# Kernel optimization log

Measured on AMD Instinct MI355X. Metric: run time of the kernel, lower is better.

## Reference

```python
import jax, jax.numpy as jnp
import numpy as np

D = 64        # GatedGraphConv out_channels
N_LAYERS = 5  # number of stacked convs


def setup_inputs() -> dict:
    key = jax.random.key(0)
    ks = jax.random.split(key, 16)
    N, E, G = 100000, 1600000, 64
    s = 0.1
    inp = {
        'conv_weight': jax.random.normal(ks[0], (N_LAYERS, D, D), jnp.float32) * s,
        'gru_w_ih':    jax.random.normal(ks[1], (N_LAYERS, 3 * D, D), jnp.float32) * s,
        'gru_w_hh':    jax.random.normal(ks[2], (N_LAYERS, 3 * D, D), jnp.float32) * s,
        'gru_b_ih':    jax.random.normal(ks[3], (N_LAYERS, 3 * D), jnp.float32) * s,
        'gru_b_hh':    jax.random.normal(ks[4], (N_LAYERS, 3 * D), jnp.float32) * s,
        'fc1_w': jax.random.normal(ks[5], (32, D), jnp.float32) * s,
        'fc1_b': jax.random.normal(ks[6], (32,), jnp.float32) * s,
        'fc2_w': jax.random.normal(ks[7], (16, 32), jnp.float32) * s,
        'fc2_b': jax.random.normal(ks[8], (16,), jnp.float32) * s,
        'fc3_w': jax.random.normal(ks[9], (1, 16), jnp.float32) * s,
        'fc3_b': jax.random.normal(ks[10], (1,), jnp.float32) * s,
        'edge_index': jax.random.randint(ks[11], (2, E), 0, N, jnp.int64 if jax.config.jax_enable_x64 else jnp.int32),
        'batch': jnp.sort(jax.random.randint(ks[12], (N,), 0, G, jnp.int32)),
        'num_nodes': N,
        'num_graphs': G,
    }
    return inp


def _gru_cell(m, h, w_ih, w_hh, b_ih, b_hh):
    # torch.nn.GRUCell math; m: [N,D] input, h: [N,D] hidden
    gi = m @ w_ih.T + b_ih   # [N, 3D]
    gh = h @ w_hh.T + b_hh   # [N, 3D]
    i_r, i_z, i_n = jnp.split(gi, 3, axis=1)
    h_r, h_z, h_n = jnp.split(gh, 3, axis=1)
    r = jax.nn.sigmoid(i_r + h_r)
    z = jax.nn.sigmoid(i_z + h_z)
    n = jnp.tanh(i_n + r * h_n)
    return (1.0 - z) * n + z * h


def reference(conv_weight, gru_w_ih, gru_w_hh, gru_b_ih, gru_b_hh,
              fc1_w, fc1_b, fc2_w, fc2_b, fc3_w, fc3_b,
              edge_index, batch, num_nodes, num_graphs):
    src, dst = edge_index[0], edge_index[1]  # source_to_target flow
    # initial node features: zeros [N,8] zero-padded to D by GatedGraphConv
    x0 = jnp.zeros((num_nodes, D), jnp.float32)

    def step(x, params):
        w, wih, whh, bih, bhh = params
        m = x @ w                                        # [N, D]
        agg = jax.ops.segment_sum(m[src], dst, num_segments=num_nodes)  # scatter-add
        return _gru_cell(agg, x, wih, whh, bih, bhh), None

    x, _ = jax.lax.scan(step, x0,
                        (conv_weight, gru_w_ih, gru_w_hh, gru_b_ih, gru_b_hh))

    # scatter_add pooling over batch -> [num_graphs, D]
    g = jax.ops.segment_sum(x, batch, num_segments=num_graphs)
    h = jax.nn.elu(g @ fc1_w.T + fc1_b)
    h = jax.nn.elu(h @ fc2_w.T + fc2_b)
    return h @ fc3_w.T + fc3_b  # [num_graphs, 1]
```

## Files before the change

kernel.cpp:

```cpp
#include <hip/hip_runtime.h>
#include <math.h>

typedef _Float16 f16x2 __attribute__((ext_vector_type(2)));
typedef _Float16 f16x4 __attribute__((ext_vector_type(4)));
typedef _Float16 f16x8 __attribute__((ext_vector_type(8)));
typedef float f32x4 __attribute__((ext_vector_type(4)));

#define CBITS 10
#define FCHUNK 4096
#define MATSZ 13056
#define SEGSZ 2176
__device__ __forceinline__ int woff(int row) { return 64 * row + 8 * (row >> 1); }

__device__ __forceinline__ float sigmoidf_(float v) {
  return 1.0f / (1.0f + __expf(-v));
}
__device__ __forceinline__ float tanhf_(float v) {
  v = fminf(fmaxf(v, -15.f), 15.f);
  float e = __expf(2.f * v);
  return (e - 1.f) / (e + 1.f);
}
__device__ __forceinline__ float eluf_(float v) { return v > 0.f ? v : (__expf(v) - 1.f); }

__global__ __launch_bounds__(256) void fuse_w_kernel(const float* __restrict__ conv_w,
                                                     const float* __restrict__ w_ih,
                                                     _Float16* __restrict__ wcS) {
  const int l = blockIdx.x >> 2;
  const int j0 = (blockIdx.x & 3) * 48;
  const float* W = conv_w + (size_t)l * 4096;
  const float* wi = w_ih + (size_t)l * 12288;
  _Float16* out = wcS + (size_t)l * MATSZ;
  __shared__ float sWt[64 * 68];
  __shared__ float sI[48 * 64];
  const int t = threadIdx.x;
  for (int i = t; i < 4096; i += 256) sWt[(i & 63) * 68 + (i >> 6)] = W[i];
  for (int i = t; i < 3072; i += 256) sI[i] = wi[j0 * 64 + i];
  __syncthreads();
#pragma unroll
  for (int r = 0; r < 3; ++r) {
    int u = t + 256 * r;
    int j = u >> 4, cg = (u & 15) * 4;
    float4 a = {0.f, 0.f, 0.f, 0.f};
    for (int k = 0; k < 64; ++k) {
      float4 w = *(const float4*)(sWt + k * 68 + cg);
      float s = sI[j * 64 + k];
      a.x += w.x * s; a.y += w.y * s; a.z += w.z * s; a.w += w.w * s;
    }
    int row = j0 + j;
    f16x4 hv;
    hv[0] = (_Float16)a.x; hv[1] = (_Float16)a.y;
    hv[2] = (_Float16)a.z; hv[3] = (_Float16)a.w;
    *(f16x4*)(out + woff(row) + cg) = hv;
  }
}

__global__ __launch_bounds__(256) void whh_prep_kernel(const float* __restrict__ whh,
                                                       _Float16* __restrict__ whhS) {
  int idx = blockIdx.x * 256 + threadIdx.x;
  if (idx >= 15360) return;
  int l = idx / 3072, rem = idx % 3072;
  int r = rem >> 4, c4 = (rem & 15) * 4;
  float4 v = *(const float4*)(whh + (size_t)l * 12288 + r * 64 + c4);
  f16x4 hv;
  hv[0] = (_Float16)v.x; hv[1] = (_Float16)v.y;
  hv[2] = (_Float16)v.z; hv[3] = (_Float16)v.w;
  *(f16x4*)(whhS + (size_t)l * MATSZ + woff(r) + c4) = hv;
}

__global__ __launch_bounds__(256) void bucket_hist_kernel(const int* __restrict__ dst,
                                                          int* __restrict__ bh, int E) {
  __shared__ int h[128];
  const int t = threadIdx.x;
  if (t < 128) h[t] = 0;
  __syncthreads();
  for (int e = blockIdx.x * 256 + t; e < E; e += gridDim.x * 256)
    atomicAdd(&h[dst[e] >> CBITS], 1);
  __syncthreads();
  if (t < 128 && h[t]) atomicAdd(&bh[t * 16], h[t]);
}

__global__ __launch_bounds__(128) void bucket_scan_kernel(int* __restrict__ bh, int nbk,
                                                          int* __restrict__ boffs, int E,
                                                          float* __restrict__ gbuf, int gn) {
  __shared__ int s[128];
  const int t = threadIdx.x;
  for (int i = t; i < gn; i += 128) gbuf[i] = 0.f;
  int v = (t < nbk) ? bh[t * 16] : 0;
  s[t] = v;
  __syncthreads();
  for (int o = 1; o < 128; o <<= 1) {
    int a = (t >= o) ? s[t - o] : 0;
    __syncthreads();
    s[t] += a;
    __syncthreads();
  }
  if (t < nbk) {
    int ex = s[t] - v;
    boffs[t] = ex;
    bh[t * 16] = ex;
  }
  if (t == 0) boffs[nbk] = E;
}

__global__ __launch_bounds__(256) void bucket_fill_kernel(const int* __restrict__ src,
                                                          const int* __restrict__ dst,
                                                          int* __restrict__ bcur,
                                                          unsigned* __restrict__ pairs, int E) {
  __shared__ uint2 staged[FCHUNK];
  __shared__ int h[128], lbase[128], gbase[128], lcur[128];
  const int t = threadIdx.x;
  const int e0 = blockIdx.x * FCHUNK;
  int cnt = E - e0;
  if (cnt > FCHUNK) cnt = FCHUNK;
  if (t < 128) h[t] = 0;
  __syncthreads();
  for (int i = t; i < cnt; i += 256) atomicAdd(&h[dst[e0 + i] >> CBITS], 1);
  __syncthreads();
  if (t < 128) lcur[t] = h[t];
  __syncthreads();
  for (int o = 1; o < 128; o <<= 1) {
    int a = 0;
    if (t < 128 && t >= o) a = lcur[t - o];
    __syncthreads();
    if (t < 128) lcur[t] += a;
    __syncthreads();
  }
  if (t < 128) {
    int ex = lcur[t] - h[t];
    lbase[t] = ex;
    if (h[t]) gbase[t] = atomicAdd(&bcur[t * 16], h[t]);
    lcur[t] = ex;
  }
  __syncthreads();
  for (int i = t; i < cnt; i += 256) {
    int d = dst[e0 + i];
    int b = d >> CBITS;
    int p = atomicAdd(&lcur[b], 1);
    staged[p] = make_uint2((unsigned)src[e0 + i], (unsigned)d);
  }
  __syncthreads();
  for (int i = t; i < cnt; i += 256) {
    uint2 pr = staged[i];
    int b = (int)(pr.y >> CBITS);
    pairs[gbase[b] + (i - lbase[b])] = (pr.x << CBITS) | (pr.y & ((1u << CBITS) - 1));
  }
}

__global__ __launch_bounds__(256) void csr_build_kernel(const unsigned* __restrict__ pairs,
                                                        const int* __restrict__ boffs,
                                                        int* __restrict__ offs,
                                                        int* __restrict__ srcs, int N, int E) {
  const int b = blockIdx.x, t = threadIdx.x;
  const int nbase = b << CBITS;
  __shared__ int deg[1024];
  __shared__ int ssc[256];
  for (int i = t; i < 1024; i += 256) deg[i] = 0;
  __syncthreads();
  const int beg = boffs[b], end = boffs[b + 1];
  for (int e = beg + t; e < end; e += 256) atomicAdd(&deg[pairs[e] & 1023], 1);
  __syncthreads();
  int d0 = deg[4 * t], d1 = deg[4 * t + 1], d2 = deg[4 * t + 2], d3 = deg[4 * t + 3];
  int s = d0 + d1 + d2 + d3;
  ssc[t] = s;
  __syncthreads();
  for (int o = 1; o < 256; o <<= 1) {
    int a = (t >= o) ? ssc[t - o] : 0;
    __syncthreads();
    ssc[t] += a;
    __syncthreads();
  }
  int base = beg + ssc[t] - s;
  int c0 = base, c1 = c0 + d0, c2 = c1 + d1, c3 = c2 + d2;
  if (nbase + 4 * t + 0 < N) offs[nbase + 4 * t + 0] = c0;
  if (nbase + 4 * t + 1 < N) offs[nbase + 4 * t + 1] = c1;
  if (nbase + 4 * t + 2 < N) offs[nbase + 4 * t + 2] = c2;
  if (nbase + 4 * t + 3 < N) offs[nbase + 4 * t + 3] = c3;
  deg[4 * t] = c0; deg[4 * t + 1] = c1; deg[4 * t + 2] = c2; deg[4 * t + 3] = c3;
  if (b == 0 && t == 0) offs[N] = E;
  if (b == 0 && t < 64) srcs[E + t] = 0;
  __syncthreads();
  for (int e = beg + t; e < end; e += 256) {
    unsigned p = pairs[e];
    int pos = atomicAdd(&deg[p & 1023], 1);
    srcs[pos] = (int)(p >> CBITS);
  }
}

__global__ __launch_bounds__(256) void l01_prep_kernel(const float* __restrict__ b_ih0,
                                                       const float* __restrict__ b_hh0,
                                                       const _Float16* __restrict__ wcS1,
                                                       const _Float16* __restrict__ whhS1,
                                                       const float* __restrict__ b_ih1,
                                                       const float* __restrict__ b_hh1,
                                                       float* __restrict__ h1,
                                                       float* __restrict__ u,
                                                       float* __restrict__ cons) {
  __shared__ float sh1[64];
  int j = threadIdx.x;
  if (j < 64) {
    float r = sigmoidf_(b_ih0[j] + b_hh0[j]);
    float z = sigmoidf_(b_ih0[64 + j] + b_hh0[64 + j]);
    float n = tanhf_(b_ih0[128 + j] + r * b_hh0[128 + j]);
    float h = (1.f - z) * n;
    sh1[j] = h;
    h1[j] = h;
  }
  __syncthreads();
  if (j >= 192) return;
  float su = 0.f, sg = 0.f;
  const int base = woff(j);
  for (int c = 0; c < 64; ++c) {
    float hc = sh1[c];
    su += hc * (float)wcS1[base + c];
    sg += hc * (float)whhS1[base + c];
  }
  u[j] = su;
  if (j < 128) {
    cons[j] = sg + b_ih1[j] + b_hh1[j];
  } else {
    cons[j] = b_ih1[j];
    cons[j + 64] = sg + b_hh1[j];
  }
}

__global__ __launch_bounds__(256) void l1_elem_kernel(const int* __restrict__ offs,
                                                      const float* __restrict__ h1,
                                                      const float* __restrict__ u,
                                                      const float* __restrict__ cons,
                                                      _Float16* __restrict__ xh,
                                                      int N, int units) {
  int idx = blockIdx.x * 256 + threadIdx.x;
  if (idx >= units) return;
  int v = idx >> 5, lp = idx & 31;
  float dg = (v < N) ? (float)(offs[v + 1] - offs[v]) : 0.f;
  f16x2 o;
#pragma unroll
  for (int k = 0; k < 2; ++k) {
    int d = 2 * lp + k;
    float r = sigmoidf_(dg * u[d] + cons[d]);
    float z = sigmoidf_(dg * u[64 + d] + cons[64 + d]);
    float n = tanhf_(dg * u[128 + d] + cons[128 + d] + r * cons[192 + d]);
    o[k] = (_Float16)(n + z * (h1[d] - n));
  }
  *(f16x2*)(xh + (size_t)idx * 2) = o;
}

__global__ __launch_bounds__(256) void agg_kernel(const _Float16* __restrict__ xh,
                                                  const int* __restrict__ offs,
                                                  const int* __restrict__ srcs,
                                                  _Float16* __restrict__ aggh, int N) {
  int wave = threadIdx.x >> 6, lane = threadIdx.x & 63;
  int v = blockIdx.x * 4 + wave;
  if (v >= N) return;
  const int beg = offs[v], end = offs[v + 1];
  const int deg = end - beg;
  const int og = lane >> 3;
  const int lp = lane & 7;
  f16x8 acc = {};
  for (int base = 0; base < deg; base += 64) {
    const int cnt = min(64, deg - base);
    int sidx = srcs[beg + base + lane];
    for (int e = 0; e < cnt; e += 8) {
      int me = e + og;
      int s = __shfl(sidx, me);
      f16x8 vv = *(const f16x8*)(xh + (size_t)s * 64 + lp * 8);
      if (me < cnt) acc += vv;
    }
  }
#pragma unroll
  for (int off = 8; off < 64; off <<= 1) {
    union { f16x8 h; int i[4]; } a, b;
    a.h = acc;
#pragma unroll
    for (int w = 0; w < 4; ++w) b.i[w] = __shfl_xor(a.i[w], off);
    acc += b.h;
  }
  if (og == 0) *(f16x8*)(aggh + (size_t)v * 64 + lp * 8) = acc;
}

__global__ __launch_bounds__(256) void gru_kernel(const _Float16* __restrict__ aggh,
                                                  const _Float16* __restrict__ xh_in,
                                                  _Float16* __restrict__ xh_out,
                                                  const _Float16* __restrict__ wcS,
                                                  const _Float16* __restrict__ whhS,
                                                  const float* __restrict__ b_ih,
                                                  const float* __restrict__ b_hh,
                                                  int N, int tiles) {
  __shared__ _Float16 sW[2 * 3 * SEGSZ];
  const int t = threadIdx.x;
  const int half = blockIdx.x & 1;
  for (int i = t; i < 1632; i += 256) {
    int mat = (i >= 816) ? 1 : 0;
    int rem = i - mat * 816;
    int seg = rem / 272;
    int u = rem % 272;
    const _Float16* srcp = (mat ? whhS : wcS) + woff(half * 32 + seg * 64) + u * 8;
    *(f16x8*)(sW + (mat * 3 + seg) * SEGSZ + u * 8) = *(const f16x8*)srcp;
  }
  __syncthreads();
  const int wave = t >> 6, lane = t & 63;
  const int q = lane >> 4, c = lane & 15;
  float bRZ[2], bZZ[2], bIN[2], bHN[2];
#pragma unroll
  for (int p = 0; p < 2; ++p) {
    int d = (half * 2 + p) * 16 + c;
    bRZ[p] = b_ih[d] + b_hh[d];
    bZZ[p] = b_ih[64 + d] + b_hh[64 + d];
    bIN[p] = b_ih[128 + d];
    bHN[p] = b_hh[128 + d];
  }
  f16x8 idf[2];
#pragma unroll
  for (int p = 0; p < 2; ++p) {
    int tgt = p * 16 + c - q * 8;
#pragma unroll
    for (int j = 0; j < 8; ++j) idf[p][j] = (j == tgt) ? (_Float16)1.0f : (_Float16)0.0f;
  }
#pragma unroll 1
  for (int tile = blockIdx.x >> 1; tile < tiles; tile += gridDim.x >> 1) {
    const int nb0 = tile * 64 + wave * 16;
    const size_t rowbase = (size_t)(nb0 + c) * 64;
    f16x8 aA[2], aH[2];
#pragma unroll
    for (int ks = 0; ks < 2; ++ks) {
      aA[ks] = *(const f16x8*)(aggh + rowbase + ks * 32 + q * 8);
      aH[ks] = *(const f16x8*)(xh_in + rowbase + ks * 32 + q * 8);
    }
    f32x4 aR[2], aZ[2], aN[2], aHNa[2], aHO[2];
#pragma unroll
    for (int p = 0; p < 2; ++p) {
      aR[p] = (f32x4){bRZ[p], bRZ[p], bRZ[p], bRZ[p]};
      aZ[p] = (f32x4){bZZ[p], bZZ[p], bZZ[p], bZZ[p]};
      aN[p] = (f32x4){bIN[p], bIN[p], bIN[p], bIN[p]};
      aHNa[p] = (f32x4){bHN[p], bHN[p], bHN[p], bHN[p]};
      aHO[p] = (f32x4){0.f, 0.f, 0.f, 0.f};
    }
#pragma unroll
    for (int ks = 0; ks < 2; ++ks) {
      const int colo = ks * 32 + q * 8;
#pragma unroll
      for (int p = 0; p < 2; ++p) {
        const int lr = p * 16 + c;
        const int ro = 64 * lr + 8 * (lr >> 1);
        f16x8 bWr = *(const f16x8*)(sW + 0 * SEGSZ + ro + colo);
        f16x8 bWz = *(const f16x8*)(sW + 1 * SEGSZ + ro + colo);
        f16x8 bWn = *(const f16x8*)(sW + 2 * SEGSZ + ro + colo);
        f16x8 bHr = *(const f16x8*)(sW + 3 * SEGSZ + ro + colo);
        f16x8 bHz = *(const f16x8*)(sW + 4 * SEGSZ + ro + colo);
        f16x8 bHn = *(const f16x8*)(sW + 5 * SEGSZ + ro + colo);
        aR[p] = __builtin_amdgcn_mfma_f32_16x16x32_f16(aA[ks], bWr, aR[p], 0, 0, 0);
        aR[p] = __builtin_amdgcn_mfma_f32_16x16x32_f16(aH[ks], bHr, aR[p], 0, 0, 0);
        aZ[p] = __builtin_amdgcn_mfma_f32_16x16x32_f16(aA[ks], bWz, aZ[p], 0, 0, 0);
        aZ[p] = __builtin_amdgcn_mfma_f32_16x16x32_f16(aH[ks], bHz, aZ[p], 0, 0, 0);
        aN[p] = __builtin_amdgcn_mfma_f32_16x16x32_f16(aA[ks], bWn, aN[p], 0, 0, 0);
        aHNa[p] = __builtin_amdgcn_mfma_f32_16x16x32_f16(aH[ks], bHn, aHNa[p], 0, 0, 0);
      }
    }
#pragma unroll
    for (int p = 0; p < 2; ++p)
      aHO[p] = __builtin_amdgcn_mfma_f32_16x16x32_f16(aH[half], idf[p], aHO[p], 0, 0, 0);
#pragma unroll
    for (int p = 0; p < 2; ++p) {
      int d = (half * 2 + p) * 16 + c;
#pragma unroll
      for (int r = 0; r < 4; ++r) {
        int node = nb0 + q * 4 + r;
        if (node < N) {
          float rr = sigmoidf_(aR[p][r]);
          float zz = sigmoidf_(aZ[p][r]);
          float nn = tanhf_(aN[p][r] + rr * aHNa[p][r]);
          float out = nn + zz * (aHO[p][r] - nn);
          xh_out[(size_t)node * 64 + d] = (_Float16)out;
        }
      }
    }
  }
}

__global__ __launch_bounds__(256) void pool_kernel(const _Float16* __restrict__ xh,
                                                   const int* __restrict__ batch,
                                                   float* __restrict__ g, int N) {
  int wave = threadIdx.x >> 6, lane = threadIdx.x & 63;
  int n0 = blockIdx.x * 64 + wave * 16;
  if (n0 >= N) return;
  int end = n0 + 16;
  if (end > N) end = N;
  int cur = batch[n0];
  float acc = 0.f;
  for (int n = n0; n < end; ++n) {
    int b = batch[n];
    if (b != cur) {
      atomicAdd(&g[(size_t)cur * 64 + lane], acc);
      acc = 0.f;
      cur = b;
    }
    acc += (float)xh[(size_t)n * 64 + lane];
  }
  atomicAdd(&g[(size_t)cur * 64 + lane], acc);
}

__global__ __launch_bounds__(256) void mlp_kernel(const float* __restrict__ g,
                                                  const float* __restrict__ w1,
                                                  const float* __restrict__ b1,
                                                  const float* __restrict__ w2,
                                                  const float* __restrict__ b2,
                                                  const float* __restrict__ w3,
                                                  const float* __restrict__ b3,
                                                  float* __restrict__ out, int G) {
  __shared__ float sG[64 * 64];
  __shared__ float sH1[64 * 32];
  __shared__ float sH2[64 * 16];
  int t = threadIdx.x;
  for (int i = t; i < G * 64; i += 256) sG[i] = g[i];
  __syncthreads();
  for (int o = t; o < G * 32; o += 256) {
    int gi = o >> 5, i = o & 31;
    float a = b1[i];
    for (int k = 0; k < 64; ++k) a += sG[gi * 64 + k] * w1[i * 64 + k];
    sH1[gi * 32 + i] = eluf_(a);
  }
  __syncthreads();
  for (int o = t; o < G * 16; o += 256) {
    int gi = o >> 4, i = o & 15;
    float a = b2[i];
    for (int k = 0; k < 32; ++k) a += sH1[gi * 32 + k] * w2[i * 32 + k];
    sH2[gi * 16 + i] = eluf_(a);
  }
  __syncthreads();
  for (int o = t; o < G; o += 256) {
    float a = b3[0];
    for (int k = 0; k < 16; ++k) a += sH2[o * 16 + k] * w3[k];
    out[o] = a;
  }
}

extern "C" void kernel_launch(void* const* d_in, const int* in_sizes, int n_in,
                              void* d_out, int out_size, void* d_ws, size_t ws_size,
                              hipStream_t stream) {
  const float* conv_w = (const float*)d_in[0];
  const float* w_ih = (const float*)d_in[1];
  const float* w_hh = (const float*)d_in[2];
  const float* b_ih = (const float*)d_in[3];
  const float* b_hh = (const float*)d_in[4];
  const float* fc1_w = (const float*)d_in[5];
  const float* fc1_b = (const float*)d_in[6];
  const float* fc2_w = (const float*)d_in[7];
  const float* fc2_b = (const float*)d_in[8];
  const float* fc3_w = (const float*)d_in[9];
  const float* fc3_b = (const float*)d_in[10];
  const int* ei = (const int*)d_in[11];
  const int* batch = (const int*)d_in[12];
  const int N = in_sizes[12];
  const int E = in_sizes[11] / 2;
  const int G = out_size;
  const int* src = ei;
  const int* dst = ei + E;
  const int nbk = (N + 1023) >> CBITS;
  const int tiles = (N + 63) / 64;
  const int Npad = tiles * 64;

  char* ws = (char*)d_ws;
  size_t off = 0;
  auto alloc = [&](size_t bytes) -> void* {
    void* p = ws + off;
    off += (bytes + 255) & ~(size_t)255;
    return p;
  };
  _Float16* xhA = (_Float16*)alloc((size_t)Npad * 64 * 2);
  _Float16* xhB = (_Float16*)alloc((size_t)Npad * 64 * 2);
  _Float16* aggh = (_Float16*)alloc((size_t)Npad * 64 * 2);
  _Float16* wcS = (_Float16*)alloc((size_t)5 * MATSZ * 2);
  _Float16* whhS = (_Float16*)alloc((size_t)5 * MATSZ * 2);
  float* h1 = (float*)alloc(64 * 4);
  float* l1u = (float*)alloc(192 * 4);
  float* l1c = (float*)alloc(256 * 4);
  float* gbuf = (float*)alloc((size_t)G * 64 * 4);
  int* offs = (int*)alloc((size_t)(N + 1) * 4);
  int* srcs = (int*)alloc((size_t)(E + 64) * 4);
  unsigned* pairs = (unsigned*)alloc((size_t)E * 4);
  int* bh = (int*)alloc(128 * 16 * 4);
  int* boffs = (int*)alloc(129 * 4);

  hipMemsetAsync(bh, 0, 128 * 16 * 4, stream);
  bucket_hist_kernel<<<256, 256, 0, stream>>>(dst, bh, E);
  bucket_scan_kernel<<<1, 128, 0, stream>>>(bh, nbk, boffs, E, gbuf, G * 64);
  bucket_fill_kernel<<<(E + FCHUNK - 1) / FCHUNK, 256, 0, stream>>>(src, dst, bh, pairs, E);
  csr_build_kernel<<<nbk, 256, 0, stream>>>(pairs, boffs, offs, srcs, N, E);

  fuse_w_kernel<<<20, 256, 0, stream>>>(conv_w, w_ih, wcS);
  whh_prep_kernel<<<60, 256, 0, stream>>>(w_hh, whhS);

  l01_prep_kernel<<<1, 256, 0, stream>>>(b_ih, b_hh, wcS + MATSZ, whhS + MATSZ,
                                         b_ih + 192, b_hh + 192, h1, l1u, l1c);
  l1_elem_kernel<<<(Npad * 32 + 255) / 256, 256, 0, stream>>>(offs, h1, l1u, l1c, xhA,
                                                              N, Npad * 32);

  _Float16* cur = xhA;
  _Float16* nxt = xhB;
  for (int l = 2; l < 5; ++l) {
    agg_kernel<<<(N + 3) / 4, 256, 0, stream>>>(cur, offs, srcs, aggh, N);
    gru_kernel<<<768, 256, 0, stream>>>(aggh, cur, nxt, wcS + (size_t)l * MATSZ,
                                        whhS + (size_t)l * MATSZ, b_ih + (size_t)l * 192,
                                        b_hh + (size_t)l * 192, N, tiles);
    _Float16* tmp = cur; cur = nxt; nxt = tmp;
  }

  pool_kernel<<<(N + 63) / 64, 256, 0, stream>>>(cur, batch, gbuf, N);
  mlp_kernel<<<1, 256, 0, stream>>>(gbuf, fc1_w, fc1_b, fc2_w, fc2_b, fc3_w, fc3_b,
                                    (float*)d_out, G);
}
```

Baseline: 413.5 us.

## Use per-degree lookup table for layer-two state in the first aggregation

```diff
diff --git a/kernel.cpp b/kernel.cpp
--- a/kernel.cpp
+++ b/kernel.cpp
@@ -10,6 +10,7 @@
 #define FCHUNK 4096
 #define MATSZ 13056
 #define SEGSZ 2176
+#define TABN 512
 __device__ __forceinline__ int woff(int row) { return 64 * row + 8 * (row >> 1); }
 
 __device__ __forceinline__ float sigmoidf_(float v) {
@@ -149,7 +150,9 @@
 __global__ __launch_bounds__(256) void csr_build_kernel(const unsigned* __restrict__ pairs,
                                                         const int* __restrict__ boffs,
                                                         int* __restrict__ offs,
-                                                        int* __restrict__ srcs, int N, int E) {
+                                                        int* __restrict__ srcs,
+                                                        unsigned short* __restrict__ deg16,
+                                                        int N, int E) {
   const int b = blockIdx.x, t = threadIdx.x;
   const int nbase = b << CBITS;
   __shared__ int deg[1024];
@@ -171,10 +174,10 @@
   }
   int base = beg + ssc[t] - s;
   int c0 = base, c1 = c0 + d0, c2 = c1 + d1, c3 = c2 + d2;
-  if (nbase + 4 * t + 0 < N) offs[nbase + 4 * t + 0] = c0;
-  if (nbase + 4 * t + 1 < N) offs[nbase + 4 * t + 1] = c1;
-  if (nbase + 4 * t + 2 < N) offs[nbase + 4 * t + 2] = c2;
-  if (nbase + 4 * t + 3 < N) offs[nbase + 4 * t + 3] = c3;
+  if (nbase + 4 * t + 0 < N) { offs[nbase + 4 * t + 0] = c0; deg16[nbase + 4 * t + 0] = (unsigned short)d0; }
+  if (nbase + 4 * t + 1 < N) { offs[nbase + 4 * t + 1] = c1; deg16[nbase + 4 * t + 1] = (unsigned short)d1; }
+  if (nbase + 4 * t + 2 < N) { offs[nbase + 4 * t + 2] = c2; deg16[nbase + 4 * t + 2] = (unsigned short)d2; }
+  if (nbase + 4 * t + 3 < N) { offs[nbase + 4 * t + 3] = c3; deg16[nbase + 4 * t + 3] = (unsigned short)d3; }
   deg[4 * t] = c0; deg[4 * t + 1] = c1; deg[4 * t + 2] = c2; deg[4 * t + 3] = c3;
   if (b == 0 && t == 0) offs[N] = E;
   if (b == 0 && t < 64) srcs[E + t] = 0;
@@ -223,26 +226,63 @@
   }
 }
 
-__global__ __launch_bounds__(256) void l1_elem_kernel(const int* __restrict__ offs,
-                                                      const float* __restrict__ h1,
-                                                      const float* __restrict__ u,
-                                                      const float* __restrict__ cons,
-                                                      _Float16* __restrict__ xh,
-                                                      int N, int units) {
+__global__ __launch_bounds__(256) void h2tab_kernel(const float* __restrict__ h1,
+                                                    const float* __restrict__ u,
+                                                    const float* __restrict__ cons,
+                                                    _Float16* __restrict__ tab) {
+  int idx = blockIdx.x * 256 + threadIdx.x;
+  if (idx >= TABN * 64) return;
+  int dgi = idx >> 6, j = idx & 63;
+  float dg = (float)dgi;
+  float r = sigmoidf_(dg * u[j] + cons[j]);
+  float z = sigmoidf_(dg * u[64 + j] + cons[64 + j]);
+  float n = tanhf_(dg * u[128 + j] + cons[128 + j] + r * cons[192 + j]);
+  tab[idx] = (_Float16)(n + z * (h1[j] - n));
+}
+
+__global__ __launch_bounds__(256) void l1_elem_kernel(const unsigned short* __restrict__ deg16,
+                                                      const _Float16* __restrict__ tab,
+                                                      _Float16* __restrict__ xh, int units) {
   int idx = blockIdx.x * 256 + threadIdx.x;
   if (idx >= units) return;
-  int v = idx >> 5, lp = idx & 31;
-  float dg = (v < N) ? (float)(offs[v + 1] - offs[v]) : 0.f;
-  f16x2 o;
-#pragma unroll
-  for (int k = 0; k < 2; ++k) {
-    int d = 2 * lp + k;
-    float r = sigmoidf_(dg * u[d] + cons[d]);
-    float z = sigmoidf_(dg * u[64 + d] + cons[64 + d]);
-    float n = tanhf_(dg * u[128 + d] + cons[128 + d] + r * cons[192 + d]);
-    o[k] = (_Float16)(n + z * (h1[d] - n));
-  }
-  *(f16x2*)(xh + (size_t)idx * 2) = o;
+  int v = idx >> 3, lp = idx & 7;
+  int dg = min((int)deg16[v], TABN - 1);
+  *(f16x8*)(xh + (size_t)idx * 8) = *(const f16x8*)(tab + dg * 64 + lp * 8);
+}
+
+__global__ __launch_bounds__(256) void agg2_kernel(const _Float16* __restrict__ tab,
+                                                   const unsigned short* __restrict__ deg16,
+                                                   const int* __restrict__ offs,
+                                                   const int* __restrict__ srcs,
+                                                   _Float16* __restrict__ aggh, int N) {
+  int wave = threadIdx.x >> 6, lane = threadIdx.x & 63;
+  int v = blockIdx.x * 4 + wave;
+  if (v >= N) return;
+  const int beg = offs[v], end = offs[v + 1];
+  const int deg = end - beg;
+  const int og = lane >> 3;
+  const int lp = lane & 7;
+  f16x8 acc = {};
+  for (int base = 0; base < deg; base += 64) {
+    const int cnt = min(64, deg - base);
+    int sidx = srcs[beg + base + lane];
+    for (int e = 0; e < cnt; e += 8) {
+      int me = e + og;
+      int s = __shfl(sidx, me);
+      int dgs = min((int)deg16[s], TABN - 1);
+      f16x8 vv = *(const f16x8*)(tab + dgs * 64 + lp * 8);
+      if (me < cnt) acc += vv;
+    }
+  }
+#pragma unroll
+  for (int off = 8; off < 64; off <<= 1) {
+    union { f16x8 h; int i[4]; } a, b;
+    a.h = acc;
+#pragma unroll
+    for (int w = 0; w < 4; ++w) b.i[w] = __shfl_xor(a.i[w], off);
+    acc += b.h;
+  }
+  if (og == 0) *(f16x8*)(aggh + (size_t)v * 64 + lp * 8) = acc;
 }
 
 __global__ __launch_bounds__(256) void agg_kernel(const _Float16* __restrict__ xh,
@@ -471,12 +511,14 @@
   _Float16* aggh = (_Float16*)alloc((size_t)Npad * 64 * 2);
   _Float16* wcS = (_Float16*)alloc((size_t)5 * MATSZ * 2);
   _Float16* whhS = (_Float16*)alloc((size_t)5 * MATSZ * 2);
+  _Float16* h2tab = (_Float16*)alloc((size_t)TABN * 64 * 2);
   float* h1 = (float*)alloc(64 * 4);
   float* l1u = (float*)alloc(192 * 4);
   float* l1c = (float*)alloc(256 * 4);
   float* gbuf = (float*)alloc((size_t)G * 64 * 4);
   int* offs = (int*)alloc((size_t)(N + 1) * 4);
   int* srcs = (int*)alloc((size_t)(E + 64) * 4);
+  unsigned short* deg16 = (unsigned short*)alloc((size_t)Npad * 2);
   unsigned* pairs = (unsigned*)alloc((size_t)E * 4);
   int* bh = (int*)alloc(128 * 16 * 4);
   int* boffs = (int*)alloc(129 * 4);
@@ -485,19 +527,22 @@
   bucket_hist_kernel<<<256, 256, 0, stream>>>(dst, bh, E);
   bucket_scan_kernel<<<1, 128, 0, stream>>>(bh, nbk, boffs, E, gbuf, G * 64);
   bucket_fill_kernel<<<(E + FCHUNK - 1) / FCHUNK, 256, 0, stream>>>(src, dst, bh, pairs, E);
-  csr_build_kernel<<<nbk, 256, 0, stream>>>(pairs, boffs, offs, srcs, N, E);
+  csr_build_kernel<<<nbk, 256, 0, stream>>>(pairs, boffs, offs, srcs, deg16, N, E);
 
   fuse_w_kernel<<<20, 256, 0, stream>>>(conv_w, w_ih, wcS);
   whh_prep_kernel<<<60, 256, 0, stream>>>(w_hh, whhS);
 
   l01_prep_kernel<<<1, 256, 0, stream>>>(b_ih, b_hh, wcS + MATSZ, whhS + MATSZ,
                                          b_ih + 192, b_hh + 192, h1, l1u, l1c);
-  l1_elem_kernel<<<(Npad * 32 + 255) / 256, 256, 0, stream>>>(offs, h1, l1u, l1c, xhA,
-                                                              N, Npad * 32);
-
-  _Float16* cur = xhA;
-  _Float16* nxt = xhB;
-  for (int l = 2; l < 5; ++l) {
+  h2tab_kernel<<<(TABN * 64 + 255) / 256, 256, 0, stream>>>(h1, l1u, l1c, h2tab);
+  l1_elem_kernel<<<(Npad * 8 + 255) / 256, 256, 0, stream>>>(deg16, h2tab, xhA, Npad * 8);
+
+  agg2_kernel<<<(N + 3) / 4, 256, 0, stream>>>(h2tab, deg16, offs, srcs, aggh, N);
+  gru_kernel<<<768, 256, 0, stream>>>(aggh, xhA, xhB, wcS + 2 * MATSZ, whhS + 2 * MATSZ,
+                                      b_ih + 2 * 192, b_hh + 2 * 192, N, tiles);
+  _Float16* cur = xhB;
+  _Float16* nxt = xhA;
+  for (int l = 3; l < 5; ++l) {
     agg_kernel<<<(N + 3) / 4, 256, 0, stream>>>(cur, offs, srcs, aggh, N);
     gru_kernel<<<768, 256, 0, stream>>>(aggh, cur, nxt, wcS + (size_t)l * MATSZ,
                                         whhS + (size_t)l * MATSZ, b_ih + (size_t)l * 192,
```

After: 399.3 us. 3.4% less time.
